# Optimization experiments

Measured on AMD Instinct MI355X. Metric: run time of the kernel, lower is better.

## Reference

```python
import jax, jax.numpy as jnp
import numpy as np
import math

B, S, H = 8, 1024, 1024
LN_EPS = 1e-5  # assumed epsilon of create_normalization_layer('layer_norm')


def setup_inputs() -> dict:
    key = jax.random.key(0)
    ks = jax.random.split(key, 6)
    context = jax.random.normal(ks[0], (B, S, H), dtype=jnp.float32)
    mask = jnp.ones((B, 1, S), dtype=jnp.int32)
    prior = jax.random.uniform(ks[1], (B, S, S), dtype=jnp.float32)
    # LayerNorm params
    gamma = jnp.ones((H,), dtype=jnp.float32)
    beta = jnp.zeros((H,), dtype=jnp.float32)
    # Dense projections (Glorot-like init)
    scale = 1.0 / np.sqrt(H)
    Wk = jax.random.normal(ks[2], (H, H), dtype=jnp.float32) * scale
    bk = jnp.zeros((H,), dtype=jnp.float32)
    Wq = jax.random.normal(ks[3], (H, H), dtype=jnp.float32) * scale
    bq = jnp.zeros((H,), dtype=jnp.float32)
    return {"context": context, "mask": mask, "prior": prior,
            "gamma": gamma, "beta": beta, "Wk": Wk, "bk": bk, "Wq": Wq, "bq": bq}


def reference(context, mask, prior, gamma, beta, Wk, bk, Wq, bq):
    dtype = context.dtype
    s = context.shape[1]
    hs = context.shape[2]
    i = jnp.arange(s)
    adj_upper = i[:, None] == (i[None, :] - 1)          # [S,S] superdiagonal
    adj_lower = i[:, None] == (i[None, :] + 1)          # subdiagonal
    adj_mask = adj_upper | adj_lower
    pad = mask[:, 0, :].astype(bool)                    # [B,S]
    pad2d = pad[:, :, None] & pad[:, None, :]           # [B,S,S]
    final_adj = adj_mask[None, :, :] & pad2d

    # LayerNorm over last axis
    mu = jnp.mean(context, axis=-1, keepdims=True)
    var = jnp.mean(jnp.square(context - mu), axis=-1, keepdims=True)
    cn = (context - mu) * jax.lax.rsqrt(var + LN_EPS) * gamma + beta

    k = cn @ Wk + bk                                    # [B,S,H]
    q = cn @ Wq + bq
    scores = jnp.einsum('bsh,bth->bst', q, k) / math.sqrt(hs)
    scores = jnp.where(final_adj, scores, jnp.asarray(-1e9, dtype))
    neibor = jax.nn.softmax(scores, axis=-1)
    neibor = jnp.sqrt(neibor * jnp.swapaxes(neibor, 1, 2) + 1e-9)
    neibor = prior + (1.0 - prior) * neibor

    triu = i[None, :] >= i[:, None]                     # [S,S] upper incl diag
    tri = triu.astype(dtype)
    b_eye = jnp.eye(s, dtype=bool)

    t = jnp.log(neibor + 1e-9)
    t = jnp.where(adj_upper[None, :, :], t, jnp.asarray(0.0, dtype))
    t = jnp.einsum('bij,jk->bik', t, tri)               # cumulative over cols
    g = jnp.exp(jnp.einsum('ij,bjk->bik', tri, t))      # hierarchical prefix product
    keep = jnp.logical_not(jnp.logical_xor(triu, b_eye))
    g = jnp.where(keep[None, :, :], g, jnp.asarray(0.0, dtype))
    neibor_diag = jnp.where(b_eye[None, :, :], jnp.asarray(1e-9, dtype), neibor)
    g = g + jnp.swapaxes(g, 1, 2) + neibor_diag
    g = g / (jnp.sum(g, axis=-1, keepdims=True) + 1e-9)

    f2d = pad2d.astype(dtype)
    g = g * f2d
    neibor = neibor * f2d
    return g, neibor
```

## Files before the change

kernel.cpp:

```cpp
#include <hip/hip_runtime.h>
#include <hip/hip_bf16.h>

#define SB 8
#define SS 1024
#define SH 1024
#define LN_EPS 1e-5f

typedef unsigned short u16;
typedef __attribute__((ext_vector_type(8))) short bf16x8;
typedef __attribute__((ext_vector_type(4))) float f32x4;

__device__ __forceinline__ u16 f2bf(float f) {
  __hip_bfloat16 h = __float2bfloat16(f);
  return *reinterpret_cast<u16*>(&h);
}
__device__ __forceinline__ float bf2f(u16 x) {
  unsigned v = ((unsigned)x) << 16;
  return __builtin_bit_cast(float, v);
}
__device__ __forceinline__ ushort4 pack4(float a, float b, float c, float d) {
  ushort4 o;
  o.x = f2bf(a); o.y = f2bf(b); o.z = f2bf(c); o.w = f2bf(d);
  return o;
}
__device__ __forceinline__ void gld16(const void* g, void* l) {
  __builtin_amdgcn_global_load_lds(
      (const __attribute__((address_space(1))) void*)g,
      (__attribute__((address_space(3))) void*)l, 16, 0, 0);
}

#define NPT 256
#define NWB 16
#define LNB0 (NPT + NWB)

__global__ __launch_bounds__(256) void prep_pt(
    const float* __restrict__ x, const float* __restrict__ gamma,
    const float* __restrict__ beta, const float* __restrict__ Wq,
    const float* __restrict__ Wk, const float* __restrict__ bq,
    u16* __restrict__ cnb, u16* __restrict__ PT, float* __restrict__ wkbq,
    float* __restrict__ du, float* __restrict__ dd) {
  __shared__ float p1[4], p2[4];
  __shared__ u16 As[64 * 32];
  __shared__ u16 Bs[64 * 32];
  const int blk = blockIdx.x;
  const int t = threadIdx.x;
  const int wave = t >> 6, lane = t & 63;

  if (blk >= LNB0) {
    const int row = blk - LNB0;
    const float* xr = x + (size_t)row * SH;
    float4 v = *(const float4*)(xr + 4 * t);

    float s = v.x + v.y + v.z + v.w;
#pragma unroll
    for (int off = 32; off > 0; off >>= 1) s += __shfl_down(s, off, 64);
    if (lane == 0) p1[wave] = s;
    __syncthreads();
    const float mu = (p1[0] + p1[1] + p1[2] + p1[3]) * (1.0f / SH);

    float d0 = v.x - mu, d1 = v.y - mu, d2 = v.z - mu, d3 = v.w - mu;
    float ss = d0 * d0 + d1 * d1 + d2 * d2 + d3 * d3;
#pragma unroll
    for (int off = 32; off > 0; off >>= 1) ss += __shfl_down(ss, off, 64);
    if (lane == 0) p2[wave] = ss;
    __syncthreads();
    const float rstd =
        rsqrtf((p2[0] + p2[1] + p2[2] + p2[3]) * (1.0f / SH) + LN_EPS);

    float4 gm = *(const float4*)(gamma + 4 * t);
    float4 bt = *(const float4*)(beta + 4 * t);
    ushort4 o = pack4(d0 * rstd * gm.x + bt.x, d1 * rstd * gm.y + bt.y,
                      d2 * rstd * gm.z + bt.z, d3 * rstd * gm.w + bt.w);
    *(ushort4*)(cnb + (size_t)row * SH + 4 * t) = o;
    if (t == 0) {
      du[row] = 0.f;
      dd[row] = 0.f;
    }
  } else if (blk < NPT) {
    const int m0 = (blk >> 4) * 64;
    const int n0 = (blk & 15) * 64;
    const int wn = wave * 16;
    const int l15 = lane & 15, q = lane >> 4;

    f32x4 acc[4] = {};
    const int srow = t >> 2;
    const int scol = (t & 3) * 8;
    const float* gA = Wk + (size_t)(m0 + srow) * SH + scol;
    const float* gB = Wq + (size_t)(n0 + srow) * SH + scol;
    u16* lA = &As[srow * 32 + scol];
    u16* lB = &Bs[srow * 32 + scol];

    for (int k0 = 0; k0 < SH; k0 += 32) {
      float4 a0 = *(const float4*)(gA + k0);
      float4 a1 = *(const float4*)(gA + k0 + 4);
      float4 b0 = *(const float4*)(gB + k0);
      float4 b1 = *(const float4*)(gB + k0 + 4);
      __syncthreads();
      *(ushort4*)lA = pack4(a0.x, a0.y, a0.z, a0.w);
      *(ushort4*)(lA + 4) = pack4(a1.x, a1.y, a1.z, a1.w);
      *(ushort4*)lB = pack4(b0.x, b0.y, b0.z, b0.w);
      *(ushort4*)(lB + 4) = pack4(b1.x, b1.y, b1.z, b1.w);
      __syncthreads();

      bf16x8 af[4];
#pragma unroll
      for (int fm = 0; fm < 4; ++fm)
        af[fm] = *(const bf16x8*)&As[(fm * 16 + l15) * 32 + q * 8];
      bf16x8 bfr = *(const bf16x8*)&Bs[(wn + l15) * 32 + q * 8];
#pragma unroll
      for (int fm = 0; fm < 4; ++fm)
        acc[fm] = __builtin_amdgcn_mfma_f32_16x16x32_bf16(af[fm], bfr, acc[fm],
                                                          0, 0, 0);
    }

#pragma unroll
    for (int fm = 0; fm < 4; ++fm) {
      const int row0 = m0 + fm * 16 + q * 4;
      const int col = n0 + wn + l15;
#pragma unroll
      for (int r = 0; r < 4; ++r)
        PT[(size_t)(row0 + r) * SH + col] = f2bf(acc[fm][r]);
    }
  } else {
    const int rbase = (blk - NPT) * 64 + wave * 16;
    float4 bv[4];
#pragma unroll
    for (int j = 0; j < 4; ++j)
      bv[j] = *(const float4*)(bq + lane * 16 + 4 * j);
    for (int i = 0; i < 16; ++i) {
      const float* wr = Wk + (size_t)(rbase + i) * SH + lane * 16;
      float s = 0.f;
#pragma unroll
      for (int j = 0; j < 4; ++j) {
        float4 w4 = *(const float4*)(wr + 4 * j);
        s += w4.x * bv[j].x + w4.y * bv[j].y + w4.z * bv[j].z + w4.w * bv[j].w;
      }
#pragma unroll
      for (int off = 32; off > 0; off >>= 1) s += __shfl_down(s, off, 64);
      if (lane == 0) wkbq[rbase + i] = s;
    }
  }
}

#define GK 1024
#define BM 128
#define BN 128
#define BK 32

__global__ __launch_bounds__(256) void ugemm_fused(const u16* __restrict__ A,
                                                   const u16* __restrict__ Bt,
                                                   const u16* __restrict__ cnb,
                                                   const float* __restrict__ wkbq,
                                                   float* __restrict__ du,
                                                   float* __restrict__ dd) {
  __shared__ u16 As[2][BM * BK];
  __shared__ u16 Bs[2][BN * BK];
  __shared__ u16 cn_s[144 * 128];
  const int tid = threadIdx.x;
  const int swz = (blockIdx.x & 7) * 64 + (blockIdx.x >> 3);
  const int m0 = (swz >> 3) * BM;
  const int n0 = (swz & 7) * BN;
  const int wave = tid >> 6, lane = tid & 63;
  const int wm = (wave & 1) * 64, wn = (wave >> 1) * 64;
  const int l15 = lane & 15, q = lane >> 4;

  {
    const int lr4 = lane >> 4;
    const int cb = lane & 15;
#pragma unroll
    for (int rd = 0; rd < 9; ++rd) {
      const int rowbase = rd * 16 + wave * 4;
      const int rowi = rowbase + lr4;
      const int sw = (rowi >> 2) & 3;
      int gr = m0 - 1 + rowi;
      gr = max(0, min(SB * SS - 1, gr));
      gld16(cnb + (size_t)gr * SH + n0 + ((cb ^ (sw << 1)) << 3),
            &cn_s[rowbase * 128]);
    }
  }

  f32x4 acc[4][4] = {};
  const int srow = tid >> 2;
  const int scol = 8 * (tid & 3);
  const u16* gA = A + (size_t)(m0 + srow) * GK + scol;
  const u16* gB = Bt + (size_t)(n0 + srow) * GK + scol;
  const int so = srow * BK + scol;

  gld16(gA, &As[0][so]);
  gld16(gA + (size_t)64 * GK, &As[0][64 * BK + so]);
  gld16(gB, &Bs[0][so]);
  gld16(gB + (size_t)64 * GK, &Bs[0][64 * BK + so]);

  int cur = 0;
  for (int t = 0; t < 31; ++t) {
    const int k1 = (t + 1) * BK;
    u16* nA = &As[cur ^ 1][so];
    u16* nB = &Bs[cur ^ 1][so];
    gld16(gA + k1, nA);
    gld16(gA + (size_t)64 * GK + k1, nA + 64 * BK);
    gld16(gB + k1, nB);
    gld16(gB + (size_t)64 * GK + k1, nB + 64 * BK);

    asm volatile("s_waitcnt vmcnt(4)" ::: "memory");
    __builtin_amdgcn_sched_barrier(0);
    __builtin_amdgcn_s_barrier();
    __builtin_amdgcn_sched_barrier(0);

    const u16* cA = As[cur];
    const u16* cB = Bs[cur];
    bf16x8 af[4], bfr[4];
#pragma unroll
    for (int fm = 0; fm < 4; ++fm)
      af[fm] = *(const bf16x8*)&cA[(wm + fm * 16 + l15) * BK + q * 8];
#pragma unroll
    for (int fn = 0; fn < 4; ++fn)
      bfr[fn] = *(const bf16x8*)&cB[(wn + fn * 16 + l15) * BK + q * 8];
#pragma unroll
    for (int fm = 0; fm < 4; ++fm)
#pragma unroll
      for (int fn = 0; fn < 4; ++fn)
        acc[fm][fn] = __builtin_amdgcn_mfma_f32_16x16x32_bf16(
            af[fm], bfr[fn], acc[fm][fn], 0, 0, 0);

    __builtin_amdgcn_s_barrier();
    __builtin_amdgcn_sched_barrier(0);
    cur ^= 1;
  }

  asm volatile("s_waitcnt vmcnt(0)" ::: "memory");
  __builtin_amdgcn_sched_barrier(0);
  __builtin_amdgcn_s_barrier();
  __builtin_amdgcn_sched_barrier(0);
  {
    const u16* cA = As[cur];
    const u16* cB = Bs[cur];
    bf16x8 af[4], bfr[4];
#pragma unroll
    for (int fm = 0; fm < 4; ++fm)
      af[fm] = *(const bf16x8*)&cA[(wm + fm * 16 + l15) * BK + q * 8];
#pragma unroll
    for (int fn = 0; fn < 4; ++fn)
      bfr[fn] = *(const bf16x8*)&cB[(wn + fn * 16 + l15) * BK + q * 8];
#pragma unroll
    for (int fm = 0; fm < 4; ++fm)
#pragma unroll
      for (int fn = 0; fn < 4; ++fn)
        acc[fm][fn] = __builtin_amdgcn_mfma_f32_16x16x32_bf16(
            af[fm], bfr[fn], acc[fm][fn], 0, 0, 0);
  }

  float wb[4];
#pragma unroll
  for (int fn = 0; fn < 4; ++fn) wb[fn] = wkbq[n0 + wn + fn * 16 + l15];

#pragma unroll
  for (int fm = 0; fm < 4; ++fm) {
#pragma unroll
    for (int rr = 0; rr < 4; ++rr) {
      const int lr = wm + fm * 16 + q * 4 + rr;
      const int r = m0 + lr;
      const int sl = r & (SS - 1);
      const int ru = lr + 2;
      const int swu = ((ru >> 2) & 3) << 4;
      const int swd = ((lr >> 2) & 3) << 4;
      const u16* up = &cn_s[ru * 128];
      const u16* dn = &cn_s[lr * 128];
      float sdu = 0.f, sdd = 0.f;
#pragma unroll
      for (int fn = 0; fn < 4; ++fn) {
        const int lc = wn + fn * 16 + l15;
        const float a = acc[fm][fn][rr] + wb[fn];
        sdu += a * bf2f(up[lc ^ swu]);
        sdd += a * bf2f(dn[lc ^ swd]);
      }
      if (sl == SS - 1) sdu = 0.f;
      if (sl == 0) sdd = 0.f;
#pragma unroll
      for (int m = 1; m < 16; m <<= 1) {
        sdu += __shfl_xor(sdu, m, 64);
        sdd += __shfl_xor(sdd, m, 64);
      }
      if (l15 == 0) {
        atomicAdd(&du[r], sdu);
        atomicAdd(&dd[r], sdd);
      }
    }
  }
}

__device__ __forceinline__ void soft2(const float* __restrict__ du,
                                      const float* __restrict__ dd, int x,
                                      float& pu, float& pd) {
  const int sl = x & (SS - 1);
  if (sl == 0) { pu = 1.f; pd = 0.f; }
  else if (sl == SS - 1) { pu = 0.f; pd = 1.f; }
  else {
    const float a = du[x] * 0.03125f;
    const float b = dd[x] * 0.03125f;
    const float m = fmaxf(a, b);
    const float eu = __expf(a - m), ed = __expf(b - m);
    const float inv = 1.f / (eu + ed);
    pu = eu * inv;
    pd = ed * inv;
  }
}

__global__ __launch_bounds__(256) void rows_fused(const float* __restrict__ prior,
                                                  const int* __restrict__ mask,
                                                  const float* __restrict__ du,
                                                  const float* __restrict__ dd,
                                                  float* __restrict__ g_out,
                                                  float* __restrict__ ne_out) {
  const int r = blockIdx.x;
  const int b = r >> 10, i = r & (SS - 1);
  const int t = threadIdx.x;
  const int wave = t >> 6, lane = t & 63;
  const float nbz = 3.1622776601683795e-5f;

  float nb_im1 = nbz, nb_ip1 = nbz;
  if (i >= 1) {
    float pu_m, pd_m, pu_c, pd_c;
    soft2(du, dd, r - 1, pu_m, pd_m);
    soft2(du, dd, r, pu_c, pd_c);
    nb_im1 = sqrtf(pu_m * pd_c + 1e-9f);
  }
  if (i <= SS - 2) {
    float pu_c, pd_c, pu_p, pd_p;
    soft2(du, dd, r, pu_c, pd_c);
    soft2(du, dd, r + 1, pu_p, pd_p);
    nb_ip1 = sqrtf(pu_c * pd_p + 1e-9f);
  }

  const float* prow = prior + (size_t)r * SS;
  float4 pr = *(const float4*)(prow + 4 * t);
  const int* mrow = mask + b * SS;
  const float padi = (mrow[i] != 0) ? 1.f : 0.f;
  int4 mk = *(const int4*)(mrow + 4 * t);

  float ne[4], gsum = 0.f;
#pragma unroll
  for (int v = 0; v < 4; ++v) {
    const int k = 4 * t + v;
    const float p = (&pr.x)[v];
    const float nb = (k == i - 1) ? nb_im1 : (k == i + 1) ? nb_ip1 : nbz;
    const float n = p + (1.f - p) * nb;
    ne[v] = n;
    gsum += (k == i) ? (2.f + 1e-9f) : (1.f + n);
  }

  __shared__ float part[4];
#pragma unroll
  for (int off = 32; off > 0; off >>= 1) gsum += __shfl_down(gsum, off, 64);
  if (lane == 0) part[wave] = gsum;
  __syncthreads();
  const float inv = 1.f / (part[0] + part[1] + part[2] + part[3] + 1e-9f);

  float4 go, no;
#pragma unroll
  for (int v = 0; v < 4; ++v) {
    const int k = 4 * t + v;
    const float padk = ((&mk.x)[v] != 0) ? 1.f : 0.f;
    const float f2 = padi * padk;
    const float gt = (k == i) ? (2.f + 1e-9f) : (1.f + ne[v]);
    (&go.x)[v] = gt * inv * f2;
    (&no.x)[v] = ne[v] * f2;
  }
  *(float4*)(g_out + (size_t)r * SS + 4 * t) = go;
  *(float4*)(ne_out + (size_t)r * SS + 4 * t) = no;
}

extern "C" void kernel_launch(void* const* d_in, const int* in_sizes, int n_in,
                              void* d_out, int out_size, void* d_ws, size_t ws_size,
                              hipStream_t stream) {
  const float* context = (const float*)d_in[0];
  const int* mask = (const int*)d_in[1];
  const float* prior = (const float*)d_in[2];
  const float* gamma = (const float*)d_in[3];
  const float* beta = (const float*)d_in[4];
  const float* Wk = (const float*)d_in[5];
  const float* bk = (const float*)d_in[6];
  const float* Wq = (const float*)d_in[7];
  const float* bq = (const float*)d_in[8];
  (void)bk;

  float* out_g = (float*)d_out;
  float* out_n = out_g + (size_t)SB * SS * SS;

  char* ws = (char*)d_ws;
  u16* cnb = (u16*)ws;
  u16* PT = (u16*)(ws + ((size_t)16 << 20));
  float* wkbq = (float*)(ws + ((size_t)18 << 20));
  float* du = (float*)(ws + ((size_t)19 << 20));
  float* dd = (float*)(ws + ((size_t)20 << 20));

  prep_pt<<<LNB0 + SB * SS, 256, 0, stream>>>(context, gamma, beta, Wq, Wk, bq,
                                              cnb, PT, wkbq, du, dd);
  ugemm_fused<<<512, 256, 0, stream>>>(cnb, PT, cnb, wkbq, du, dd);
  rows_fused<<<SB * SS, 256, 0, stream>>>(prior, mask, du, dd, out_g, out_n);
}
```

Baseline: 189.9 us.

## Widen GEMM tile to 128x256 with 512 threads and swizzled LDS layout

Result: no change. 192.2 us (+1.2%).

```diff
diff --git a/kernel.cpp b/kernel.cpp
--- a/kernel.cpp
+++ b/kernel.cpp
@@ -144,10 +144,10 @@
 
 #define GK 1024
 #define BM 128
-#define BN 128
+#define BN 256
 #define BK 32
 
-__global__ __launch_bounds__(256) void ugemm_fused(const u16* __restrict__ A,
+__global__ __launch_bounds__(512) void ugemm_fused(const u16* __restrict__ A,
                                                    const u16* __restrict__ Bt,
                                                    const u16* __restrict__ cnb,
                                                    const float* __restrict__ wkbq,
@@ -155,53 +155,54 @@
                                                    float* __restrict__ dd) {
   __shared__ u16 As[2][BM * BK];
   __shared__ u16 Bs[2][BN * BK];
-  __shared__ u16 cn_s[144 * 128];
+  __shared__ u16 cn_s[144 * 256];
   const int tid = threadIdx.x;
-  const int swz = (blockIdx.x & 7) * 64 + (blockIdx.x >> 3);
-  const int m0 = (swz >> 3) * BM;
-  const int n0 = (swz & 7) * BN;
+  const int xcd = blockIdx.x & 7, idx = blockIdx.x >> 3;
+  const int swz = xcd * 32 + idx;
+  const int m0 = (swz >> 2) * BM;
+  const int n0 = (swz & 3) * BN;
   const int wave = tid >> 6, lane = tid & 63;
   const int wm = (wave & 1) * 64, wn = (wave >> 1) * 64;
   const int l15 = lane & 15, q = lane >> 4;
 
   {
-    const int lr4 = lane >> 4;
-    const int cb = lane & 15;
+    const int rsub = tid >> 5;
+    const int cb = tid & 31;
 #pragma unroll
     for (int rd = 0; rd < 9; ++rd) {
-      const int rowbase = rd * 16 + wave * 4;
-      const int rowi = rowbase + lr4;
-      const int sw = (rowi >> 2) & 3;
+      const int rowi = rd * 16 + rsub;
+      const int sw = ((rowi >> 2) & 3) << 1;
       int gr = m0 - 1 + rowi;
       gr = max(0, min(SB * SS - 1, gr));
-      gld16(cnb + (size_t)gr * SH + n0 + ((cb ^ (sw << 1)) << 3),
-            &cn_s[rowbase * 128]);
+      gld16(cnb + (size_t)gr * SH + n0 + ((cb ^ sw) << 3),
+            &cn_s[(rd * 16 + (wave << 1)) * 256]);
     }
   }
 
   f32x4 acc[4][4] = {};
   const int srow = tid >> 2;
-  const int scol = 8 * (tid & 3);
-  const u16* gA = A + (size_t)(m0 + srow) * GK + scol;
-  const u16* gB = Bt + (size_t)(n0 + srow) * GK + scol;
-  const int so = srow * BK + scol;
-
-  gld16(gA, &As[0][so]);
-  gld16(gA + (size_t)64 * GK, &As[0][64 * BK + so]);
-  gld16(gB, &Bs[0][so]);
-  gld16(gB + (size_t)64 * GK, &Bs[0][64 * BK + so]);
+  const int sblk = (tid & 3) ^ (srow & 3);
+  const u16* gA = A + (size_t)(m0 + srow) * GK + sblk * 8;
+  const u16* gB0 = Bt + (size_t)(n0 + srow) * GK + sblk * 8;
+  const u16* gB1 = Bt + (size_t)(n0 + 128 + srow) * GK + sblk * 8;
+  const int soA = tid * 8;
+  const int soB0 = tid * 8;
+  const int soB1 = 4096 + tid * 8;
+
+  gld16(gA, &As[0][soA]);
+  gld16(gB0, &Bs[0][soB0]);
+  gld16(gB1, &Bs[0][soB1]);
+
+  const int rsw = (q ^ (l15 & 3)) * 8;
 
   int cur = 0;
   for (int t = 0; t < 31; ++t) {
     const int k1 = (t + 1) * BK;
-    u16* nA = &As[cur ^ 1][so];
-    u16* nB = &Bs[cur ^ 1][so];
-    gld16(gA + k1, nA);
-    gld16(gA + (size_t)64 * GK + k1, nA + 64 * BK);
-    gld16(gB + k1, nB);
-    gld16(gB + (size_t)64 * GK + k1, nB + 64 * BK);
-
-    asm volatile("s_waitcnt vmcnt(4)" ::: "memory");
+    gld16(gA + k1, &As[cur ^ 1][soA]);
+    gld16(gB0 + k1, &Bs[cur ^ 1][soB0]);
+    gld16(gB1 + k1, &Bs[cur ^ 1][soB1]);
+
+    asm volatile("s_waitcnt vmcnt(3)" ::: "memory");
     __builtin_amdgcn_sched_barrier(0);
     __builtin_amdgcn_s_barrier();
     __builtin_amdgcn_sched_barrier(0);
@@ -211,10 +212,10 @@
     bf16x8 af[4], bfr[4];
 #pragma unroll
     for (int fm = 0; fm < 4; ++fm)
-      af[fm] = *(const bf16x8*)&cA[(wm + fm * 16 + l15) * BK + q * 8];
+      af[fm] = *(const bf16x8*)&cA[(wm + fm * 16 + l15) * BK + rsw];
 #pragma unroll
     for (int fn = 0; fn < 4; ++fn)
-      bfr[fn] = *(const bf16x8*)&cB[(wn + fn * 16 + l15) * BK + q * 8];
+      bfr[fn] = *(const bf16x8*)&cB[(wn + fn * 16 + l15) * BK + rsw];
 #pragma unroll
     for (int fm = 0; fm < 4; ++fm)
 #pragma unroll
@@ -237,10 +238,10 @@
     bf16x8 af[4], bfr[4];
 #pragma unroll
     for (int fm = 0; fm < 4; ++fm)
-      af[fm] = *(const bf16x8*)&cA[(wm + fm * 16 + l15) * BK + q * 8];
+      af[fm] = *(const bf16x8*)&cA[(wm + fm * 16 + l15) * BK + rsw];
 #pragma unroll
     for (int fn = 0; fn < 4; ++fn)
-      bfr[fn] = *(const bf16x8*)&cB[(wn + fn * 16 + l15) * BK + q * 8];
+      bfr[fn] = *(const bf16x8*)&cB[(wn + fn * 16 + l15) * BK + rsw];
 #pragma unroll
     for (int fm = 0; fm < 4; ++fm)
 #pragma unroll
@@ -263,8 +264,8 @@
       const int ru = lr + 2;
       const int swu = ((ru >> 2) & 3) << 4;
       const int swd = ((lr >> 2) & 3) << 4;
-      const u16* up = &cn_s[ru * 128];
-      const u16* dn = &cn_s[lr * 128];
+      const u16* up = &cn_s[ru * 256];
+      const u16* dn = &cn_s[lr * 256];
       float sdu = 0.f, sdd = 0.f;
 #pragma unroll
       for (int fn = 0; fn < 4; ++fn) {
@@ -395,6 +396,6 @@
 
   prep_pt<<<LNB0 + SB * SS, 256, 0, stream>>>(context, gamma, beta, Wq, Wk, bq,
                                               cnb, PT, wkbq, du, dd);
-  ugemm_fused<<<512, 256, 0, stream>>>(cnb, PT, cnb, wkbq, du, dd);
+  ugemm_fused<<<256, 512, 0, stream>>>(cnb, PT, cnb, wkbq, du, dd);
   rows_fused<<<SB * SS, 256, 0, stream>>>(prior, mask, du, dd, out_g, out_n);
 }
```
